# Performance work log

Measured on AMD Instinct MI355X. Metric: run time of the kernel, lower is better.

Reference implementation:

```python
import jax, jax.numpy as jnp
import numpy as np

B, S, D = 8, 2048, 1024
N = 256          # state_dim
H = 512          # selector_hidden
E = 8            # num_experts


def murmurhash3_finalizer(token_ids):
    # Torch code works in int64 but masks to 32 bits after each multiply and
    # values stay non-negative, so it is exactly uint32 wrapping arithmetic.
    x = token_ids.astype(jnp.uint32)
    x = x ^ (x >> 16)
    x = x * jnp.uint32(2246822507)
    x = x ^ (x >> 13)
    x = x * jnp.uint32(3266489909)
    x = x ^ (x >> 16)
    return x


def setup_inputs() -> dict:
    key = jax.random.key(0)
    ks = jax.random.split(key, 7)
    scale = 0.02
    return {
        "x": jax.random.normal(ks[0], (B, S, D), dtype=jnp.float32),
        "token_ids": jax.random.randint(ks[1], (B, S), 0, 50257, dtype=jnp.int32),
        "Win": jax.random.normal(ks[2], (E, N, D), dtype=jnp.float32) * scale,      # in_proj.weight per expert
        "Wsin": jax.random.normal(ks[3], (E, H, D), dtype=jnp.float32) * scale,     # selector_in.weight
        "Wsout": jax.random.normal(ks[4], (E, 4 * N, H), dtype=jnp.float32) * scale,  # selector_out.weight
        "Wout": jax.random.normal(ks[5], (E, D, N), dtype=jnp.float32) * scale,     # out_proj.weight
        "dparam": jnp.ones((E, N), dtype=jnp.float32),                              # per-expert d
    }


def _forward(x, Win, Wsin, Wsout, Wout, dparam, token_ids):
    b, s, d = x.shape
    e_num, n, _ = Win.shape
    routes = (murmurhash3_finalizer(token_ids) % jnp.uint32(e_num)).astype(jnp.int32)  # (B,S)

    # Per-token expert projections, selected by hash route (masked accumulation
    # over the small fixed expert count; honors per-token routing).
    u = jnp.zeros((b, s, n), x.dtype)
    a = jnp.zeros((b, s, n), x.dtype)
    bg = jnp.zeros((b, s, n), x.dtype)
    c = jnp.zeros((b, s, n), x.dtype)
    dg = jnp.zeros((b, s, n), x.dtype)
    for e in range(e_num):
        m = (routes == e)[..., None]
        u = jnp.where(m, jnp.einsum('bsd,nd->bsn', x, Win[e]), u)
        sh = jax.nn.silu(jnp.einsum('bsd,hd->bsh', x, Wsin[e]))
        sel = jnp.einsum('bsh,oh->bso', sh, Wsout[e])       # (B,S,4N)
        ar, br, cr, dr = jnp.split(sel, 4, axis=-1)
        a = jnp.where(m, jax.nn.sigmoid(ar), a)
        bg = jnp.where(m, jnp.tanh(br), bg)
        c = jnp.where(m, jnp.tanh(cr), c)
        dg = jnp.where(m, jax.nn.sigmoid(dr), dg)

    dvec = dparam[routes]              # (B,S,N) expert d param per token
    skip = dvec * dg * u               # residual term, state-independent

    bidx = jnp.arange(b)

    def step(states, inp):
        # states: (B,E,N) per-expert hidden state per batch row
        route_t, u_t, a_t, b_t, c_t, skip_t = inp
        h_prev = states[bidx, route_t]                 # (B,N)
        h = a_t * h_prev + b_t * u_t
        states = states.at[bidx, route_t].set(h)       # only routed expert updates
        y = c_t * h + skip_t
        return states, y

    xs = (routes.swapaxes(0, 1), u.swapaxes(0, 1), a.swapaxes(0, 1),
          bg.swapaxes(0, 1), c.swapaxes(0, 1), skip.swapaxes(0, 1))
    states0 = jnp.zeros((b, e_num, n), x.dtype)
    _, ys = jax.lax.scan(step, states0, xs)            # ys: (S,B,N)
    y = ys.swapaxes(0, 1)                              # (B,S,N)

    out = jnp.zeros((b, s, d), x.dtype)
    for e in range(e_num):
        m = (routes == e)[..., None]
        out = jnp.where(m, jnp.einsum('bsn,dn->bsd', y, Wout[e]), out)
    return out


def reference(x, token_ids, Win, Wsin, Wsout, Wout, dparam):
    return _forward(x, Win, Wsin, Wsout, Wout, dparam, token_ids)
```

## Files before the change

kernel.cpp:

```cpp
#include <hip/hip_runtime.h>


#define TOKS 16384
#define RPAD 16512
#define DD   1024
#define NN   256
#define HH   512
#define MAXTILES  136
#define MAXCHUNKS 1088
#define CHUNK 16
#define CVTBLKS 12288

typedef short short8 __attribute__((ext_vector_type(8)));
typedef float floatx4 __attribute__((ext_vector_type(4)));
typedef _Float16 half_t;

#define AS_GLOBAL __attribute__((address_space(1)))
#define AS_LDS    __attribute__((address_space(3)))

__device__ __forceinline__ void gl_lds16(const void* g, void* l) {
    __builtin_amdgcn_global_load_lds((const AS_GLOBAL void*)g, (AS_LDS void*)l, 16, 0, 0);
}

__device__ __forceinline__ unsigned short f2bf(float f) {
    union { float f; unsigned u; } c; c.f = f;
    unsigned r = c.u + 0x7FFF + ((c.u >> 16) & 1);
    return (unsigned short)(r >> 16);
}
__device__ __forceinline__ int route_of(int token) {
    unsigned x = (unsigned)token;
    x ^= x >> 16; x *= 2246822507u; x ^= x >> 13; x *= 3266489909u; x ^= x >> 16;
    return (int)(x & 7u);
}
__device__ __forceinline__ float sigm(float v) { return 1.0f / (1.0f + __expf(-v)); }
__device__ __forceinline__ float ftanh(float v) {
    float e = __expf(2.0f * v);
    return 1.0f - 2.0f / (e + 1.0f);
}

union H2 { unsigned u; half_t h[2]; };

__global__ void k_route(const int* __restrict__ tok, int* __restrict__ cnt) {
    int b = blockIdx.x, tid = threadIdx.x;
    __shared__ int lc[256 * 8];
    #pragma unroll
    for (int e = 0; e < 8; e++) lc[tid * 8 + e] = 0;
    #pragma unroll
    for (int i = 0; i < 8; i++) {
        int e = route_of(tok[b * 2048 + tid * 8 + i]);
        lc[tid * 8 + e]++;
    }
    __syncthreads();
    if (tid < 8) {
        int s = 0;
        for (int t = 0; t < 256; t++) s += lc[t * 8 + tid];
        cnt[b * 8 + tid] = s;
    }
}

__global__ void k_offsets(const int* __restrict__ cnt, int* __restrict__ grpoff,
                          int* __restrict__ tileE, int* __restrict__ tileS,
                          int* __restrict__ tileR,
                          int* __restrict__ cGrp, int* __restrict__ cStart,
                          int* __restrict__ cLen, int* __restrict__ gBase,
                          int* __restrict__ meta) {
    __shared__ int sc[64], ce[8], eoff[9], etile[9], gb[65], go[64];
    int tid = threadIdx.x;
    if (tid < 64) sc[tid] = cnt[tid];
    __syncthreads();
    if (tid < 8) { int s = 0; for (int b = 0; b < 8; b++) s += sc[b * 8 + tid]; ce[tid] = s; }
    __syncthreads();
    if (tid == 0) {
        eoff[0] = 0; etile[0] = 0;
        for (int e = 0; e < 8; e++) {
            eoff[e + 1] = eoff[e] + ce[e];
            etile[e + 1] = etile[e] + (ce[e] + 127) / 128;
        }
        meta[0] = etile[8];
        gb[0] = 0;
        for (int g = 0; g < 64; g++) gb[g + 1] = gb[g] + (sc[g] + CHUNK - 1) / CHUNK;
        meta[1] = gb[64];
    }
    __syncthreads();
    if (tid < 64) {
        int b = tid >> 3, e = tid & 7;
        int run = eoff[e];
        for (int b2 = 0; b2 < b; b2++) run += sc[b2 * 8 + e];
        go[tid] = run;
        grpoff[tid] = run;
    }
    __syncthreads();
    if (tid < 8) {
        int e = tid, st = eoff[e], c = ce[e], t0 = etile[e];
        for (int i = 0, k = 0; i < c; i += 128, k++) {
            tileE[t0 + k] = e; tileS[t0 + k] = st + i;
            tileR[t0 + k] = (c - i < 128) ? (c - i) : 128;
        }
    }
    if (tid < 64) {
        int g = tid, n = sc[g], base = gb[g], s0 = go[g];
        gBase[g] = base;
        for (int i = 0, c = 0; i < n; i += CHUNK, c++) {
            cGrp[base + c] = g;
            cStart[base + c] = s0 + i;
            cLen[base + c] = (n - i < CHUNK) ? (n - i) : CHUNK;
        }
    }
}

__global__ void k_scatter(const int* __restrict__ tok, const int* __restrict__ grpoff,
                          int* __restrict__ perm) {
    int b = blockIdx.x, tid = threadIdx.x;
    int lane = tid & 63, w = tid >> 6;
    __shared__ unsigned wsum[4][4];
    int r[8];
    int myc[8] = {0,0,0,0,0,0,0,0};
    #pragma unroll
    for (int i = 0; i < 8; i++) {
        int e = route_of(tok[b * 2048 + tid * 8 + i]);
        r[i] = e; myc[e]++;
    }
    unsigned p[4], v[4];
    #pragma unroll
    for (int k = 0; k < 4; k++) {
        p[k] = (unsigned)myc[2 * k] | ((unsigned)myc[2 * k + 1] << 16);
        v[k] = p[k];
    }
    #pragma unroll
    for (int off = 1; off < 64; off <<= 1) {
        #pragma unroll
        for (int k = 0; k < 4; k++) {
            unsigned o = __shfl_up(v[k], off, 64);
            if (lane >= off) v[k] += o;
        }
    }
    if (lane == 63) {
        #pragma unroll
        for (int k = 0; k < 4; k++) wsum[w][k] = v[k];
    }
    __syncthreads();
    unsigned add[4] = {0, 0, 0, 0};
    for (int ww = 0; ww < w; ww++)
        #pragma unroll
        for (int k = 0; k < 4; k++) add[k] += wsum[ww][k];
    int basep[8];
    #pragma unroll
    for (int e = 0; e < 8; e++) {
        unsigned ex = v[e >> 1] + add[e >> 1] - p[e >> 1];
        basep[e] = grpoff[b * 8 + e] + (int)((e & 1) ? (ex >> 16) : (ex & 0xffffu));
    }
    #pragma unroll
    for (int i = 0; i < 8; i++) {
        int e = r[i];
        perm[basep[e]++] = b * 2048 + tid * 8 + i;
    }
}

__global__ void k_prep(const float* __restrict__ Win, const float* __restrict__ Wsin,
                       const float* __restrict__ Wsout, const float* __restrict__ Wout,
                       unsigned short* __restrict__ W12, unsigned short* __restrict__ Wso,
                       unsigned short* __restrict__ Wo,
                       const float* __restrict__ x, const int* __restrict__ perm,
                       unsigned short* __restrict__ Xs, unsigned short* __restrict__ SHb,
                       unsigned short* __restrict__ Yb) {
    int blk = blockIdx.x, tid = threadIdx.x;
    if (blk < CVTBLKS) {
        const int C12 = 8 * 768 * 1024 / 4, CSO = 8 * 1024 * 512 / 4, CWO = 8 * 1024 * 256 / 4;
        int c = blk * 256 + tid;
        float4 v; unsigned short* dst;
        if (c < C12) {
            int d = c * 4;
            int e = d / (768 * 1024);
            int rem = d - e * (768 * 1024);
            int r = rem >> 10, k = rem & 1023;
            const float* src = (r < 256) ? (Win + (((size_t)e * 256 + r) << 10) + k)
                                         : (Wsin + (((size_t)e * 512 + (r - 256)) << 10) + k);
            v = *(const float4*)src;
            dst = W12 + d;
        } else if (c < C12 + CSO) {
            int d = (c - C12) * 4;
            v = *(const float4*)(Wsout + d);
            dst = Wso + d;
        } else {
            int d = (c - C12 - CSO) * 4;
            v = *(const float4*)(Wout + d);
            dst = Wo + d;
        }
        ushort4 o;
        o.x = f2bf(v.x); o.y = f2bf(v.y); o.z = f2bf(v.z); o.w = f2bf(v.w);
        *(ushort4*)dst = o;
    } else {
        int r = blk - CVTBLKS;
        if (r < TOKS) {
            int tok = perm[r];
            float4 v = *(const float4*)(x + (size_t)tok * 1024 + tid * 4);
            ushort4 o;
            o.x = f2bf(v.x); o.y = f2bf(v.y); o.z = f2bf(v.z); o.w = f2bf(v.w);
            *(ushort4*)(Xs + (size_t)r * 1024 + tid * 4) = o;
        } else {
            ushort4 z = {0, 0, 0, 0};
            *(ushort4*)(Xs + (size_t)r * 1024 + tid * 4) = z;
            if (tid < 128) *(ushort4*)(SHb + (size_t)r * 512 + tid * 4) = z;
            if (tid < 64)  *(ushort4*)(Yb + (size_t)r * 256 + tid * 4) = z;
        }
    }
}

template<int MODE, int KD>
__global__ __launch_bounds__(256, 4)
void k_mfma(const unsigned short* __restrict__ A, const unsigned short* __restrict__ Bw,
            const int* __restrict__ perm, const float* __restrict__ dparam,
            half_t* __restrict__ Ub, unsigned short* __restrict__ SHb,
            half_t* __restrict__ AW, half_t* __restrict__ CS,
            float* __restrict__ out,
            const int* __restrict__ tileE, const int* __restrict__ tileS,
            const int* __restrict__ tileR, const int* __restrict__ meta) {
    const int mt = blockIdx.x;
    if (mt >= meta[0]) return;
    const int e = tileE[mt], pos0 = tileS[mt], rows = tileR[mt];
    const int col0 = blockIdx.y * 64;
    const int tid = threadIdx.x;
    const int w = tid >> 6, lane = tid & 63, quad = lane >> 4, l15 = lane & 15;
    const int wm = w & 1, wn = w >> 1;
    constexpr int NOUT = (MODE == 0) ? 768 : 1024;
    constexpr int NK = KD / 32;

    __shared__ unsigned short As[3][128 * 32];
    __shared__ unsigned short Bs[3][64 * 32];

    const int r0 = tid >> 2;
    const int c8s = ((tid & 3) ^ ((tid >> 3) & 3)) * 8;
    const unsigned short* ga = A + (size_t)(pos0 + r0) * KD + c8s;
    const unsigned short* gb = Bw + ((size_t)e * NOUT + col0 + r0) * KD + c8s;

    const int sq = (quad ^ ((l15 >> 1) & 3)) * 8;
    int aoff[4], boff[2];
    #pragma unroll
    for (int i = 0; i < 4; i++) aoff[i] = (wm * 64 + i * 16 + l15) * 32 + sq;
    #pragma unroll
    for (int j = 0; j < 2; j++) boff[j] = (wn * 32 + j * 16 + l15) * 32 + sq;

    floatx4 acc[4][2] = {};

    #define STAGE(buf, k0) do { \
        gl_lds16(ga + (k0),                    As[buf] + w * 512); \
        gl_lds16(ga + (size_t)64 * KD + (k0),  As[buf] + 2048 + w * 512); \
        gl_lds16(gb + (k0),                    Bs[buf] + w * 512); \
    } while (0)

    STAGE(0, 0);
    STAGE(1, 32);
    int cur = 0, pre = 2;
    for (int kt = 0; kt < NK; kt++) {
        if (kt < NK - 1) {
            asm volatile("s_waitcnt vmcnt(3)" ::: "memory");
        } else {
            asm volatile("s_waitcnt vmcnt(0)" ::: "memory");
        }
        __builtin_amdgcn_s_barrier();
        asm volatile("" ::: "memory");
        if (kt + 2 < NK) STAGE(pre, (kt + 2) * 32);
        short8 af[4], bf[2];
        #pragma unroll
        for (int i = 0; i < 4; i++) af[i] = *(const short8*)(As[cur] + aoff[i]);
        #pragma unroll
        for (int j = 0; j < 2; j++) bf[j] = *(const short8*)(Bs[cur] + boff[j]);
        __builtin_amdgcn_s_setprio(1);
        #pragma unroll
        for (int i = 0; i < 4; i++)
            #pragma unroll
            for (int j = 0; j < 2; j++)
                acc[i][j] = __builtin_amdgcn_mfma_f32_16x16x32_bf16(af[i], bf[j], acc[i][j], 0, 0, 0);
        __builtin_amdgcn_s_setprio(0);
        asm volatile("s_waitcnt lgkmcnt(0)" ::: "memory");
        __builtin_amdgcn_sched_barrier(0);
        cur = (cur == 2) ? 0 : cur + 1;
        pre = (pre == 2) ? 0 : pre + 1;
    }
    #undef STAGE
    asm volatile("" ::: "memory");

    #pragma unroll
    for (int i = 0; i < 4; i++) {
        #pragma unroll
        for (int r = 0; r < 4; r++) {
            int m = wm * 64 + i * 16 + quad * 4 + r;
            if (m >= rows) continue;
            size_t row = (size_t)(pos0 + m);
            if (MODE == 0) {
                if (col0 < 256) {
                    #pragma unroll
                    for (int j = 0; j < 2; j++) {
                        int n = col0 + wn * 32 + j * 16 + l15;
                        Ub[row * 256 + n] = (half_t)acc[i][j][r];
                    }
                } else {
                    #pragma unroll
                    for (int j = 0; j < 2; j++) {
                        int n = col0 - 256 + wn * 32 + j * 16 + l15;
                        float v = acc[i][j][r];
                        SHb[row * 512 + n] = f2bf(v * sigm(v));
                    }
                }
            } else if (MODE == 1) {
                int region = col0 >> 8;
                #pragma unroll
                for (int j = 0; j < 2; j++) {
                    int n0 = (col0 & 255) + wn * 32 + j * 16 + l15;
                    float v = acc[i][j][r];
                    size_t rb = row * 512 + (size_t)n0 * 2;
                    if (region == 0) {
                        AW[rb] = (half_t)sigm(v);
                    } else if (region == 1) {
                        AW[rb + 1] = (half_t)(ftanh(v) * (float)Ub[row * 256 + n0]);
                    } else if (region == 2) {
                        CS[rb] = (half_t)ftanh(v);
                    } else {
                        CS[rb + 1] = (half_t)(dparam[e * 256 + n0] * sigm(v) * (float)Ub[row * 256 + n0]);
                    }
                }
            } else {
                int tok = perm[row];
                #pragma unroll
                for (int j = 0; j < 2; j++) {
                    int n = col0 + wn * 32 + j * 16 + l15;
                    out[(size_t)tok * 1024 + n] = acc[i][j][r];
                }
            }
        }
    }
}

__global__ void k_scanA(const half_t* __restrict__ AW,
                        const int* __restrict__ cStart, const int* __restrict__ cLen,
                        const int* __restrict__ meta,
                        float* __restrict__ SA, float* __restrict__ SQ) {
    int id = blockIdx.x;
    if (id >= meta[1]) return;
    int t = threadIdx.x;
    int s0 = cStart[id], L = cLen[id];
    const unsigned* AW32 = (const unsigned*)AW;
    size_t idx = (size_t)s0 * 256 + t;
    float p = 1.0f, q = 0.0f;
    for (int i = 0; i < L; i++) {
        H2 cv; cv.u = AW32[idx];
        float a = (float)cv.h[0], ww = (float)cv.h[1];
        q = a * q + ww;
        p *= a;
        idx += 256;
    }
    SA[(size_t)id * 256 + t] = p;
    SQ[(size_t)id * 256 + t] = q;
}

__global__ void k_scanB(const float* __restrict__ SA, const float* __restrict__ SQ,
                        const int* __restrict__ gBase, const int* __restrict__ cnt,
                        float* __restrict__ Hin) {
    int g = blockIdx.x, t = threadIdx.x;
    int base = gBase[g], nch = (cnt[g] + CHUNK - 1) / CHUNK;
    float h = 0.0f;
    for (int c = 0; c < nch; c++) {
        size_t k = (size_t)(base + c) * 256 + t;
        Hin[k] = h;
        h = SA[k] * h + SQ[k];
    }
}

__global__ void k_scanC(const half_t* __restrict__ AW, const half_t* __restrict__ CS,
                        const int* __restrict__ cStart, const int* __restrict__ cLen,
                        const int* __restrict__ meta, const float* __restrict__ Hin,
                        unsigned short* __restrict__ Yb) {
    int id = blockIdx.x;
    if (id >= meta[1]) return;
    int t = threadIdx.x;
    int s0 = cStart[id], L = cLen[id];
    const unsigned* AW32 = (const unsigned*)AW;
    const unsigned* CS32 = (const unsigned*)CS;
    float h = Hin[(size_t)id * 256 + t];
    size_t idx = (size_t)s0 * 256 + t;
    for (int i = 0; i < L; i++) {
        H2 av; av.u = AW32[idx];
        H2 cv; cv.u = CS32[idx];
        float a = (float)av.h[0], ww = (float)av.h[1];
        float c = (float)cv.h[0], sk = (float)cv.h[1];
        h = a * h + ww;
        Yb[idx] = f2bf(c * h + sk);
        idx += 256;
    }
}

extern "C" void kernel_launch(void* const* d_in, const int* in_sizes, int n_in,
                              void* d_out, int out_size, void* d_ws, size_t ws_size,
                              hipStream_t stream) {
    const float* xin   = (const float*)d_in[0];
    const int*   tok   = (const int*)d_in[1];
    const float* Win   = (const float*)d_in[2];
    const float* Wsin  = (const float*)d_in[3];
    const float* Wsout = (const float*)d_in[4];
    const float* Wout  = (const float*)d_in[5];
    const float* dpar  = (const float*)d_in[6];
    float* out = (float*)d_out;

    size_t off = 0;
    char* base = (char*)d_ws;
    auto alloc = [&](size_t bytes) -> void* {
        void* p = base + off;
        off += (bytes + 255) & ~(size_t)255;
        return p;
    };
    half_t*         Ub  = (half_t*)alloc((size_t)RPAD * NN * 2);
    unsigned short* SHb = (unsigned short*)alloc((size_t)RPAD * HH * 2);
    unsigned short* Xs  = (unsigned short*)alloc((size_t)RPAD * DD * 2);
    unsigned short* Yb  = (unsigned short*)alloc((size_t)RPAD * NN * 2);
    half_t* AW = (half_t*)alloc((size_t)TOKS * NN * 4);
    half_t* CS = (half_t*)alloc((size_t)TOKS * NN * 4);
    unsigned short* W12 = (unsigned short*)alloc((size_t)8 * 768 * 1024 * 2);
    unsigned short* Wso = (unsigned short*)alloc((size_t)8 * 1024 * 512 * 2);
    unsigned short* Wo  = (unsigned short*)alloc((size_t)8 * 1024 * 256 * 2);
    float* SA  = (float*)alloc((size_t)MAXCHUNKS * 256 * 4);
    float* SQ  = (float*)alloc((size_t)MAXCHUNKS * 256 * 4);
    float* Hin = (float*)alloc((size_t)MAXCHUNKS * 256 * 4);
    int* perm   = (int*)alloc(TOKS * 4);
    int* cnt    = (int*)alloc(64 * 4);
    int* grpoff = (int*)alloc(64 * 4);
    int* tileE  = (int*)alloc(MAXTILES * 4);
    int* tileS  = (int*)alloc(MAXTILES * 4);
    int* tileR  = (int*)alloc(MAXTILES * 4);
    int* cGrp   = (int*)alloc(MAXCHUNKS * 4);
    int* cStart = (int*)alloc(MAXCHUNKS * 4);
    int* cLen   = (int*)alloc(MAXCHUNKS * 4);
    int* gBase  = (int*)alloc(64 * 4);
    int* meta   = (int*)alloc(16 * 4);

    k_route<<<8, 256, 0, stream>>>(tok, cnt);
    k_offsets<<<1, 256, 0, stream>>>(cnt, grpoff, tileE, tileS, tileR,
                                     cGrp, cStart, cLen, gBase, meta);
    k_scatter<<<8, 256, 0, stream>>>(tok, grpoff, perm);
    k_prep<<<CVTBLKS + RPAD, 256, 0, stream>>>(Win, Wsin, Wsout, Wout, W12, Wso, Wo,
                                               xin, perm, Xs, SHb, Yb);

    k_mfma<0, 1024><<<dim3(MAXTILES, 12), 256, 0, stream>>>(Xs, W12, perm, dpar,
        Ub, SHb, AW, CS, out, tileE, tileS, tileR, meta);
    k_mfma<1, 512><<<dim3(MAXTILES, 16), 256, 0, stream>>>(SHb, Wso, perm, dpar,
        Ub, SHb, AW, CS, out, tileE, tileS, tileR, meta);

    k_scanA<<<MAXCHUNKS, 256, 0, stream>>>(AW, cStart, cLen, meta, SA, SQ);
    k_scanB<<<64, 256, 0, stream>>>(SA, SQ, gBase, cnt, Hin);
    k_scanC<<<MAXCHUNKS, 256, 0, stream>>>(AW, CS, cStart, cLen, meta, Hin, Yb);

    k_mfma<2, 256><<<dim3(MAXTILES, 16), 256, 0, stream>>>(Yb, Wo, perm, dpar,
        Ub, SHb, AW, CS, out, tileE, tileS, tileR, meta);
}
```

Before: 336.5 us.

## Split interleaved scan gate buffers into planar arrays and double scan chunk length

```diff
diff --git a/kernel.cpp b/kernel.cpp
--- a/kernel.cpp
+++ b/kernel.cpp
@@ -7,8 +7,8 @@
 #define NN   256
 #define HH   512
 #define MAXTILES  136
-#define MAXCHUNKS 1088
-#define CHUNK 16
+#define MAXCHUNKS 576
+#define CHUNK 32
 #define CVTBLKS 12288
 
 typedef short short8 __attribute__((ext_vector_type(8)));
@@ -37,8 +37,6 @@
     float e = __expf(2.0f * v);
     return 1.0f - 2.0f / (e + 1.0f);
 }
-
-union H2 { unsigned u; half_t h[2]; };
 
 __global__ void k_route(const int* __restrict__ tok, int* __restrict__ cnt) {
     int b = blockIdx.x, tid = threadIdx.x;
@@ -165,7 +163,7 @@
                        unsigned short* __restrict__ Yb) {
     int blk = blockIdx.x, tid = threadIdx.x;
     if (blk < CVTBLKS) {
-        const int C12 = 8 * 768 * 1024 / 4, CSO = 8 * 1024 * 512 / 4, CWO = 8 * 1024 * 256 / 4;
+        const int C12 = 8 * 768 * 1024 / 4, CSO = 8 * 1024 * 512 / 4;
         int c = blk * 256 + tid;
         float4 v; unsigned short* dst;
         if (c < C12) {
@@ -211,7 +209,8 @@
 void k_mfma(const unsigned short* __restrict__ A, const unsigned short* __restrict__ Bw,
             const int* __restrict__ perm, const float* __restrict__ dparam,
             half_t* __restrict__ Ub, unsigned short* __restrict__ SHb,
-            half_t* __restrict__ AW, half_t* __restrict__ CS,
+            half_t* __restrict__ Aa, half_t* __restrict__ Wg,
+            half_t* __restrict__ Cc, half_t* __restrict__ Sk,
             float* __restrict__ out,
             const int* __restrict__ tileE, const int* __restrict__ tileS,
             const int* __restrict__ tileR, const int* __restrict__ meta) {
@@ -307,16 +306,16 @@
                 #pragma unroll
                 for (int j = 0; j < 2; j++) {
                     int n0 = (col0 & 255) + wn * 32 + j * 16 + l15;
+                    size_t idx = row * 256 + (size_t)n0;
                     float v = acc[i][j][r];
-                    size_t rb = row * 512 + (size_t)n0 * 2;
                     if (region == 0) {
-                        AW[rb] = (half_t)sigm(v);
+                        Aa[idx] = (half_t)sigm(v);
                     } else if (region == 1) {
-                        AW[rb + 1] = (half_t)(ftanh(v) * (float)Ub[row * 256 + n0]);
+                        Wg[idx] = (half_t)(ftanh(v) * (float)Ub[idx]);
                     } else if (region == 2) {
-                        CS[rb] = (half_t)ftanh(v);
+                        Cc[idx] = (half_t)ftanh(v);
                     } else {
-                        CS[rb + 1] = (half_t)(dparam[e * 256 + n0] * sigm(v) * (float)Ub[row * 256 + n0]);
+                        Sk[idx] = (half_t)(dparam[e * 256 + n0] * sigm(v) * (float)Ub[idx]);
                     }
                 }
             } else {
@@ -331,7 +330,7 @@
     }
 }
 
-__global__ void k_scanA(const half_t* __restrict__ AW,
+__global__ void k_scanA(const half_t* __restrict__ Aa, const half_t* __restrict__ Wg,
                         const int* __restrict__ cStart, const int* __restrict__ cLen,
                         const int* __restrict__ meta,
                         float* __restrict__ SA, float* __restrict__ SQ) {
@@ -339,12 +338,10 @@
     if (id >= meta[1]) return;
     int t = threadIdx.x;
     int s0 = cStart[id], L = cLen[id];
-    const unsigned* AW32 = (const unsigned*)AW;
     size_t idx = (size_t)s0 * 256 + t;
     float p = 1.0f, q = 0.0f;
     for (int i = 0; i < L; i++) {
-        H2 cv; cv.u = AW32[idx];
-        float a = (float)cv.h[0], ww = (float)cv.h[1];
+        float a = (float)Aa[idx], ww = (float)Wg[idx];
         q = a * q + ww;
         p *= a;
         idx += 256;
@@ -366,7 +363,8 @@
     }
 }
 
-__global__ void k_scanC(const half_t* __restrict__ AW, const half_t* __restrict__ CS,
+__global__ void k_scanC(const half_t* __restrict__ Aa, const half_t* __restrict__ Wg,
+                        const half_t* __restrict__ Cc, const half_t* __restrict__ Sk,
                         const int* __restrict__ cStart, const int* __restrict__ cLen,
                         const int* __restrict__ meta, const float* __restrict__ Hin,
                         unsigned short* __restrict__ Yb) {
@@ -374,15 +372,11 @@
     if (id >= meta[1]) return;
     int t = threadIdx.x;
     int s0 = cStart[id], L = cLen[id];
-    const unsigned* AW32 = (const unsigned*)AW;
-    const unsigned* CS32 = (const unsigned*)CS;
     float h = Hin[(size_t)id * 256 + t];
     size_t idx = (size_t)s0 * 256 + t;
     for (int i = 0; i < L; i++) {
-        H2 av; av.u = AW32[idx];
-        H2 cv; cv.u = CS32[idx];
-        float a = (float)av.h[0], ww = (float)av.h[1];
-        float c = (float)cv.h[0], sk = (float)cv.h[1];
+        float a = (float)Aa[idx], ww = (float)Wg[idx];
+        float c = (float)Cc[idx], sk = (float)Sk[idx];
         h = a * h + ww;
         Yb[idx] = f2bf(c * h + sk);
         idx += 256;
@@ -412,8 +406,10 @@
     unsigned short* SHb = (unsigned short*)alloc((size_t)RPAD * HH * 2);
     unsigned short* Xs  = (unsigned short*)alloc((size_t)RPAD * DD * 2);
     unsigned short* Yb  = (unsigned short*)alloc((size_t)RPAD * NN * 2);
-    half_t* AW = (half_t*)alloc((size_t)TOKS * NN * 4);
-    half_t* CS = (half_t*)alloc((size_t)TOKS * NN * 4);
+    half_t* Aa = (half_t*)alloc((size_t)TOKS * NN * 2);
+    half_t* Wg = (half_t*)alloc((size_t)TOKS * NN * 2);
+    half_t* Cc = (half_t*)alloc((size_t)TOKS * NN * 2);
+    half_t* Sk = (half_t*)alloc((size_t)TOKS * NN * 2);
     unsigned short* W12 = (unsigned short*)alloc((size_t)8 * 768 * 1024 * 2);
     unsigned short* Wso = (unsigned short*)alloc((size_t)8 * 1024 * 512 * 2);
     unsigned short* Wo  = (unsigned short*)alloc((size_t)8 * 1024 * 256 * 2);
@@ -440,14 +436,14 @@
                                                xin, perm, Xs, SHb, Yb);
 
     k_mfma<0, 1024><<<dim3(MAXTILES, 12), 256, 0, stream>>>(Xs, W12, perm, dpar,
-        Ub, SHb, AW, CS, out, tileE, tileS, tileR, meta);
+        Ub, SHb, Aa, Wg, Cc, Sk, out, tileE, tileS, tileR, meta);
     k_mfma<1, 512><<<dim3(MAXTILES, 16), 256, 0, stream>>>(SHb, Wso, perm, dpar,
-        Ub, SHb, AW, CS, out, tileE, tileS, tileR, meta);
-
-    k_scanA<<<MAXCHUNKS, 256, 0, stream>>>(AW, cStart, cLen, meta, SA, SQ);
+        Ub, SHb, Aa, Wg, Cc, Sk, out, tileE, tileS, tileR, meta);
+
+    k_scanA<<<MAXCHUNKS, 256, 0, stream>>>(Aa, Wg, cStart, cLen, meta, SA, SQ);
     k_scanB<<<64, 256, 0, stream>>>(SA, SQ, gBase, cnt, Hin);
-    k_scanC<<<MAXCHUNKS, 256, 0, stream>>>(AW, CS, cStart, cLen, meta, Hin, Yb);
+    k_scanC<<<MAXCHUNKS, 256, 0, stream>>>(Aa, Wg, Cc, Sk, cStart, cLen, meta, Hin, Yb);
 
     k_mfma<2, 256><<<dim3(MAXTILES, 16), 256, 0, stream>>>(Yb, Wo, perm, dpar,
-        Ub, SHb, AW, CS, out, tileE, tileS, tileR, meta);
-}
+        Ub, SHb, Aa, Wg, Cc, Sk, out, tileE, tileS, tileR, meta);
+}
```

Result: no change. 336.2 us (-0.1%).
